# Kernel optimization log

Hardware: AMD Instinct MI355X
Metric: run time of the kernel (lower is better)

The kernel has to match this reference:

```python
import jax, jax.numpy as jnp
import numpy as np

E, T_MAX, H, L, V = 384, 256, 6, 6, 65
DH = E // H  # 64
EPS = 1e-5


def setup_inputs() -> dict:
    key = jax.random.key(0)
    ks = jax.random.split(key, 24)
    B, T = 128, 256
    s = 0.02
    inp = {
        "input_indices": jax.random.randint(ks[0], (B, T), 0, V, dtype=jnp.int64) if jax.config.read("jax_enable_x64") else jax.random.randint(ks[0], (B, T), 0, V, dtype=jnp.int32),
        "targets": jax.random.randint(ks[1], (B, T), 0, V, dtype=jnp.int32),
        "tok_emb": s * jax.random.normal(ks[2], (V, E), jnp.float32),
        "pos_emb": s * jax.random.normal(ks[3], (T_MAX, E), jnp.float32),
        "Wq": s * jax.random.normal(ks[4], (L, H, E, DH), jnp.float32),
        "Wk": s * jax.random.normal(ks[5], (L, H, E, DH), jnp.float32),
        "Wv": s * jax.random.normal(ks[6], (L, H, E, DH), jnp.float32),
        "Wo": s * jax.random.normal(ks[7], (L, E, E), jnp.float32),
        "bo": jnp.zeros((L, E), jnp.float32),
        "ln1_s": jnp.ones((L, E), jnp.float32),
        "ln1_b": jnp.zeros((L, E), jnp.float32),
        "ln2_s": jnp.ones((L, E), jnp.float32),
        "ln2_b": jnp.zeros((L, E), jnp.float32),
        "W1": s * jax.random.normal(ks[8], (L, E, 4 * E), jnp.float32),
        "b1": jnp.zeros((L, 4 * E), jnp.float32),
        "W2": s * jax.random.normal(ks[9], (L, 4 * E, E), jnp.float32),
        "b2": jnp.zeros((L, E), jnp.float32),
        "lnf_s": jnp.ones((E,), jnp.float32),
        "lnf_b": jnp.zeros((E,), jnp.float32),
        "Wout": s * jax.random.normal(ks[10], (E, V), jnp.float32),
        "bout": jnp.zeros((V,), jnp.float32),
    }
    return inp


def _ln(x, s, b):
    m = x.mean(-1, keepdims=True)
    v = ((x - m) ** 2).mean(-1, keepdims=True)
    return (x - m) * jax.lax.rsqrt(v + EPS) * s + b


def _forward(input_indices, targets, tok_emb, pos_emb, Wq, Wk, Wv, Wo, bo,
             ln1_s, ln1_b, ln2_s, ln2_b, W1, b1, W2, b2, lnf_s, lnf_b, Wout, bout):
    B, T = input_indices.shape
    x = tok_emb[input_indices] + pos_emb[:T]  # [B,T,E]
    causal = jnp.tril(jnp.ones((T, T), bool))
    scale = DH ** -0.5

    def block(x, p):
        wq, wk, wv, wo, bo_, l1s, l1b, l2s, l2b, w1, b1_, w2, b2_ = p
        h = _ln(x, l1s, l1b)
        q = jnp.einsum("bte,hed->bhtd", h, wq)
        k = jnp.einsum("bte,hed->bhtd", h, wk)
        v = jnp.einsum("bte,hed->bhtd", h, wv)
        scores = jnp.einsum("bhtd,bhsd->bhts", q, k) * scale
        scores = jnp.where(causal, scores, -jnp.inf)
        w = jax.nn.softmax(scores, axis=-1)
        att = jnp.einsum("bhts,bhsd->bhtd", w, v)  # [B,H,T,DH]
        att = att.transpose(0, 2, 1, 3).reshape(B, T, E)  # concat heads
        x = x + att @ wo + bo_
        h2 = _ln(x, l2s, l2b)
        ff = jax.nn.relu(h2 @ w1 + b1_) @ w2 + b2_
        return x + ff, None

    x, _ = jax.lax.scan(block, x, (Wq, Wk, Wv, Wo, bo, ln1_s, ln1_b, ln2_s, ln2_b, W1, b1, W2, b2))
    x = _ln(x, lnf_s, lnf_b)
    logits = x @ Wout + bout  # [B,T,V]
    logp = jax.nn.log_softmax(logits, axis=-1)
    nll = -jnp.take_along_axis(logp, targets[..., None], axis=-1)[..., 0]
    loss = nll.mean()
    return logits, loss


def reference(input_indices, targets, tok_emb, pos_emb, Wq, Wk, Wv, Wo, bo,
              ln1_s, ln1_b, ln2_s, ln2_b, W1, b1, W2, b2, lnf_s, lnf_b, Wout, bout):
    return _forward(input_indices, targets, tok_emb, pos_emb, Wq, Wk, Wv, Wo, bo,
                    ln1_s, ln1_b, ln2_s, ln2_b, W1, b1, W2, b2, lnf_s, lnf_b, Wout, bout)
```

## Files before the change

### kernel.cpp

```cpp
#include <hip/hip_runtime.h>

#define BT      32768
#define T_SEQ   256
#define E_DIM   384
#define NH      6
#define NL      6
#define VOC     65
#define FF_DIM  1536
#define QKV_N   1152

typedef short bf16x8 __attribute__((ext_vector_type(8)));
typedef float f32x4  __attribute__((ext_vector_type(4)));
typedef unsigned short u16;

typedef const unsigned int __attribute__((address_space(1))) gu32;
typedef unsigned int       __attribute__((address_space(3))) lu32;

__device__ __forceinline__ u16 f2bf(float x) {
  unsigned u = __builtin_bit_cast(unsigned, x);
  u += 0x7fffu + ((u >> 16) & 1u);
  return (u16)(u >> 16);
}
__device__ __forceinline__ float bf2f(u16 v) {
  unsigned u = ((unsigned)v) << 16;
  return __builtin_bit_cast(float, u);
}

__device__ __forceinline__ void load_lds_16(const void* g, void* l) {
  __builtin_amdgcn_global_load_lds((gu32*)g, (lu32*)l, 16, 0, 0);
}

__global__ __launch_bounds__(256) void transpose_t(
    const float* __restrict__ src, u16* __restrict__ dst, int R, int C,
    long sbs, long dbs_outer, int inner, long dbs_inner, long dbase) {
  __shared__ float t[32][33];
  const int b = blockIdx.z;
  const float* s = src + (long)b * sbs;
  u16* d = dst + dbase + (long)(b / inner) * dbs_outer + (long)(b % inner) * dbs_inner;
  const int r0 = blockIdx.x * 32, c0 = blockIdx.y * 32;
  const int tx = threadIdx.x & 31, ty = threadIdx.x >> 5;
#pragma unroll
  for (int i = 0; i < 4; i++) {
    int rr = ty + i * 8;
    int r = r0 + rr, c = c0 + tx;
    if (r < R && c < C) t[rr][tx] = s[(long)r * C + c];
  }
  __syncthreads();
#pragma unroll
  for (int i = 0; i < 4; i++) {
    int cc = ty + i * 8;
    int c = c0 + cc, r = r0 + tx;
    if (c < C && r < R) d[(long)c * R + r] = f2bf(t[tx][cc]);
  }
}

__global__ __launch_bounds__(256) void embed_k(const int* __restrict__ idx,
                                               const float* __restrict__ tok,
                                               const float* __restrict__ pos,
                                               u16* __restrict__ x) {
  int i = blockIdx.x * 256 + threadIdx.x;
  int bt = i / 48, q = i - bt * 48;
  int t = bt & 255;
  const float4* tp = (const float4*)(tok + (size_t)idx[bt] * E_DIM + q * 8);
  const float4* pp = (const float4*)(pos + (size_t)t * E_DIM + q * 8);
  float4 a0 = tp[0], a1 = tp[1], p0 = pp[0], p1 = pp[1];
  u16 o[8];
  o[0] = f2bf(a0.x + p0.x); o[1] = f2bf(a0.y + p0.y);
  o[2] = f2bf(a0.z + p0.z); o[3] = f2bf(a0.w + p0.w);
  o[4] = f2bf(a1.x + p1.x); o[5] = f2bf(a1.y + p1.y);
  o[6] = f2bf(a1.z + p1.z); o[7] = f2bf(a1.w + p1.w);
  *(bf16x8*)(x + (size_t)bt * E_DIM + q * 8) = *(bf16x8*)o;
}

__global__ __launch_bounds__(256) void ln_k(const u16* __restrict__ x,
                                            const float* __restrict__ gam,
                                            const float* __restrict__ bet,
                                            u16* __restrict__ out) {
  int tid = threadIdx.x, lane = tid & 63, w = tid >> 6;
  size_t token = (size_t)blockIdx.x * 4 + w;
  const u16* xr = x + token * E_DIM;
  u16 raw[6];
  *(uint2*)raw          = *(const uint2*)(xr + 4 * lane);
  *(unsigned*)(raw + 4) = *(const unsigned*)(xr + 256 + 2 * lane);
  float v[6]; float s = 0.f;
#pragma unroll
  for (int i = 0; i < 6; i++) { v[i] = bf2f(raw[i]); s += v[i]; }
#pragma unroll
  for (int d = 1; d < 64; d <<= 1) s += __shfl_xor(s, d);
  float mean = s * (1.f / E_DIM);
  float q = 0.f;
#pragma unroll
  for (int i = 0; i < 6; i++) { float d0 = v[i] - mean; q += d0 * d0; }
#pragma unroll
  for (int d = 1; d < 64; d <<= 1) q += __shfl_xor(q, d);
  float r = rsqrtf(q * (1.f / E_DIM) + 1e-5f);
  int e[6] = {4 * lane, 4 * lane + 1, 4 * lane + 2, 4 * lane + 3,
              256 + 2 * lane, 256 + 2 * lane + 1};
  u16 o[6];
#pragma unroll
  for (int i = 0; i < 6; i++)
    o[i] = f2bf((v[i] - mean) * r * gam[e[i]] + bet[e[i]]);
  u16* orow = out + token * E_DIM;
  *(uint2*)(orow + 4 * lane)          = *(uint2*)o;
  *(unsigned*)(orow + 256 + 2 * lane) = *(unsigned*)(o + 4);
}

__global__ __launch_bounds__(256) void gemm_d(
    const u16* __restrict__ A, const u16* __restrict__ Bt, int K, int Nstore,
    const float* __restrict__ bias, const u16* __restrict__ resid,
    u16* __restrict__ outH, float* __restrict__ outF, int relu) {
  __shared__ u16 smem[16384];
  u16* As = smem;
  u16* Bs = smem + 8192;
  const int tid = threadIdx.x, lane = tid & 63, wv = tid >> 6;
  const int quad = lane >> 4, l16 = lane & 15;
  const int m0 = blockIdx.x * 128, n0 = blockIdx.y * 128;
  const int wm = (wv & 1) * 64, wn = (wv >> 1) * 64;

  const int lrow = lane >> 2;
  const int lchunk = (lane & 3) ^ (lrow & 3);
  const int rs = quad == 0 ? 0 : quad;

  f32x4 acc[4][4];
#pragma unroll
  for (int i = 0; i < 4; i++)
#pragma unroll
    for (int j = 0; j < 4; j++) acc[i][j] = (f32x4){0.f, 0.f, 0.f, 0.f};

  auto stage = [&](int sel, int k0) {
#pragma unroll
    for (int j = 0; j < 2; j++) {
      int rid = wv * 2 + j;
      int r = rid * 16 + lrow;
      load_lds_16(A + (size_t)(m0 + r) * K + k0 + lchunk * 8, &As[sel * 4096 + rid * 512]);
      load_lds_16(Bt + (size_t)(n0 + r) * K + k0 + lchunk * 8, &Bs[sel * 4096 + rid * 512]);
    }
  };

  const int NK = K >> 5;
  stage(0, 0);
  __syncthreads();
  for (int kt = 0; kt < NK; kt++) {
    const int cur = kt & 1;
    if (kt + 1 < NK) stage(cur ^ 1, (kt + 1) * 32);
    const u16* Ab = As + cur * 4096;
    const u16* Bb = Bs + cur * 4096;
    const int slot = (quad ^ (l16 & 3)) * 8;
    bf16x8 af[4], bfr[4];
#pragma unroll
    for (int i = 0; i < 4; i++) af[i]  = *(const bf16x8*)&Ab[(wm + i * 16 + l16) * 32 + slot];
#pragma unroll
    for (int j = 0; j < 4; j++) bfr[j] = *(const bf16x8*)&Bb[(wn + j * 16 + l16) * 32 + slot];
#pragma unroll
    for (int i = 0; i < 4; i++)
#pragma unroll
      for (int j = 0; j < 4; j++)
        acc[i][j] = __builtin_amdgcn_mfma_f32_16x16x32_bf16(af[i], bfr[j], acc[i][j], 0, 0, 0);
    __syncthreads();
  }

  if (outH) {
#pragma unroll
    for (int p = 0; p < 4; p++) {
      if (p) __syncthreads();
      if ((wv >> 1) == (p >> 1)) {
#pragma unroll
        for (int jj = 0; jj < 2; jj++) {
          int j = (p & 1) * 2 + jj;
          int gn = n0 + wn + j * 16 + l16;
          float bv = bias ? bias[gn] : 0.f;
          int lcol = jj * 16 + l16;
#pragma unroll
          for (int i = 0; i < 4; i++)
#pragma unroll
            for (int r = 0; r < 4; r++) {
              float v = acc[i][j][r] + bv;
              if (relu) v = fmaxf(v, 0.f);
              smem[(wm + i * 16 + quad * 4 + r) * 36 + lcol] = f2bf(v);
            }
        }
      }
      __syncthreads();
      const int gc0 = n0 + p * 32;
#pragma unroll
      for (int s = 0; s < 4; s++) {
        int row = s * 32 + (tid >> 3);
        int seg = (tid & 7) * 4;
        u16 pk[4];
        *(uint2*)pk = *(const uint2*)&smem[row * 36 + seg];
        size_t o = (size_t)(m0 + row) * Nstore + gc0 + seg;
        if (resid) {
          u16 rv[4];
          *(uint2*)rv = *(const uint2*)&resid[o];
#pragma unroll
          for (int q2 = 0; q2 < 4; q2++) pk[q2] = f2bf(bf2f(pk[q2]) + bf2f(rv[q2]));
        }
        *(uint2*)&outH[o] = *(uint2*)pk;
      }
    }
  } else {
#pragma unroll
    for (int j = 0; j < 4; j++) {
      const int gn = n0 + wn + j * 16 + l16;
      if (gn < Nstore) {
        const float bv = bias ? bias[gn] : 0.f;
#pragma unroll
        for (int i = 0; i < 4; i++)
#pragma unroll
          for (int r = 0; r < 4; r++) {
            const int gm = m0 + wm + i * 16 + quad * 4 + r;
            outF[(size_t)gm * Nstore + gn] = acc[i][j][r] + bv;
          }
      }
    }
  }
}

__global__ __launch_bounds__(512) void attn_k(const u16* __restrict__ qkv,
                                              u16* __restrict__ att) {
  __shared__ u16 Kc[64 * 64];
  __shared__ u16 Vtc[64 * 64];
  __shared__ u16 Pl[8 * 32 * 64];
  const int b = blockIdx.x / NH, h = blockIdx.x % NH;
  const int tid = threadIdx.x, lane = tid & 63, w = tid >> 6;
  const int quad = lane >> 4, l16 = lane & 15;
  const int rowb = b * T_SEQ;

  bf16x8 qf[2][2];
#pragma unroll
  for (int mi = 0; mi < 2; mi++)
#pragma unroll
    for (int kk = 0; kk < 2; kk++)
      qf[mi][kk] = *(const bf16x8*)(qkv + (size_t)(rowb + w * 32 + mi * 16 + l16) * QKV_N +
                                    h * 64 + kk * 32 + quad * 8);

  f32x4 Oa[2][4];
  float mrun[2][4], lrun[2][4];
#pragma unroll
  for (int mi = 0; mi < 2; mi++) {
#pragma unroll
    for (int di = 0; di < 4; di++) Oa[mi][di] = (f32x4){0.f, 0.f, 0.f, 0.f};
#pragma unroll
    for (int r = 0; r < 4; r++) { mrun[mi][r] = -1e30f; lrun[mi][r] = 0.f; }
  }

  u16* Pw = &Pl[w * 2048];
  const int nch = (w >> 1) + 1;
  const int sr = tid >> 3, sseg = (tid & 7) * 8;

  for (int c = 0; c < 4; c++) {
    const int s0 = c * 64;
    __syncthreads();
    *(uint4*)&Kc[sr * 64 + sseg] =
        *(const uint4*)(qkv + (size_t)(rowb + s0 + sr) * QKV_N + 384 + h * 64 + sseg);
    {
      union { uint4 u; u16 us[8]; } tb;
      tb.u = *(const uint4*)(qkv + (size_t)(rowb + s0 + sr) * QKV_N + 768 + h * 64 + sseg);
#pragma unroll
      for (int j = 0; j < 8; j++) Vtc[(sseg + j) * 64 + sr] = tb.us[j];
    }
    __syncthreads();
    if (c >= nch) continue;

    f32x4 S[2][4];
    bf16x8 kf[4][2];
#pragma unroll
    for (int ni = 0; ni < 4; ni++)
#pragma unroll
      for (int kk = 0; kk < 2; kk++)
        kf[ni][kk] = *(const bf16x8*)&Kc[(ni * 16 + l16) * 64 + kk * 32 + quad * 8];
#pragma unroll
    for (int mi = 0; mi < 2; mi++)
#pragma unroll
      for (int ni = 0; ni < 4; ni++) {
        f32x4 z = (f32x4){0.f, 0.f, 0.f, 0.f};
        z = __builtin_amdgcn_mfma_f32_16x16x32_bf16(qf[mi][0], kf[ni][0], z, 0, 0, 0);
        S[mi][ni] = __builtin_amdgcn_mfma_f32_16x16x32_bf16(qf[mi][1], kf[ni][1], z, 0, 0, 0);
      }
    const bool diag = (c == nch - 1);
#pragma unroll
    for (int mi = 0; mi < 2; mi++)
#pragma unroll
      for (int ni = 0; ni < 4; ni++)
#pragma unroll
        for (int r = 0; r < 4; r++) {
          float xv = S[mi][ni][r] * 0.125f;
          if (diag) {
            int t = w * 32 + mi * 16 + quad * 4 + r;
            int s = s0 + ni * 16 + l16;
            if (s > t) xv = -1e30f;
          }
          S[mi][ni][r] = xv;
        }
#pragma unroll
    for (int mi = 0; mi < 2; mi++)
#pragma unroll
      for (int r = 0; r < 4; r++) {
        float mx = fmaxf(fmaxf(S[mi][0][r], S[mi][1][r]), fmaxf(S[mi][2][r], S[mi][3][r]));
        mx = fmaxf(mx, __shfl_xor(mx, 1));
        mx = fmaxf(mx, __shfl_xor(mx, 2));
        mx = fmaxf(mx, __shfl_xor(mx, 4));
        mx = fmaxf(mx, __shfl_xor(mx, 8));
        float mnew = fmaxf(mrun[mi][r], mx);
        float alpha = __expf(mrun[mi][r] - mnew);
        float ls = 0.f;
#pragma unroll
        for (int ni = 0; ni < 4; ni++) {
          float p = __expf(S[mi][ni][r] - mnew);
          S[mi][ni][r] = p; ls += p;
        }
        ls += __shfl_xor(ls, 1); ls += __shfl_xor(ls, 2);
        ls += __shfl_xor(ls, 4); ls += __shfl_xor(ls, 8);
        lrun[mi][r] = lrun[mi][r] * alpha + ls;
        mrun[mi][r] = mnew;
#pragma unroll
        for (int di = 0; di < 4; di++) Oa[mi][di][r] *= alpha;
      }
#pragma unroll
    for (int mi = 0; mi < 2; mi++)
#pragma unroll
      for (int ni = 0; ni < 4; ni++)
#pragma unroll
        for (int r = 0; r < 4; r++)
          Pw[(mi * 16 + quad * 4 + r) * 64 + ni * 16 + l16] = f2bf(S[mi][ni][r]);
    bf16x8 pf[2][2], vf[4][2];
#pragma unroll
    for (int mi = 0; mi < 2; mi++)
#pragma unroll
      for (int kk = 0; kk < 2; kk++)
        pf[mi][kk] = *(const bf16x8*)&Pw[(mi * 16 + l16) * 64 + kk * 32 + quad * 8];
#pragma unroll
    for (int di = 0; di < 4; di++)
#pragma unroll
      for (int kk = 0; kk < 2; kk++)
        vf[di][kk] = *(const bf16x8*)&Vtc[(di * 16 + l16) * 64 + kk * 32 + quad * 8];
#pragma unroll
    for (int mi = 0; mi < 2; mi++)
#pragma unroll
      for (int di = 0; di < 4; di++) {
        Oa[mi][di] = __builtin_amdgcn_mfma_f32_16x16x32_bf16(pf[mi][0], vf[di][0], Oa[mi][di], 0, 0, 0);
        Oa[mi][di] = __builtin_amdgcn_mfma_f32_16x16x32_bf16(pf[mi][1], vf[di][1], Oa[mi][di], 0, 0, 0);
      }
  }

#pragma unroll
  for (int mi = 0; mi < 2; mi++)
#pragma unroll
    for (int r = 0; r < 4; r++) {
      float inv = 1.f / lrun[mi][r];
      int t = w * 32 + mi * 16 + quad * 4 + r;
#pragma unroll
      for (int di = 0; di < 4; di++)
        att[(size_t)(rowb + t) * E_DIM + h * 64 + di * 16 + l16] = f2bf(Oa[mi][di][r] * inv);
    }
}

__global__ __launch_bounds__(256) void loss_k(const float* __restrict__ logits,
                                              const int* __restrict__ tgt,
                                              float* __restrict__ loss) {
  __shared__ float part[4];
  const int tid = threadIdx.x, lane = tid & 63, w = tid >> 6;
  const int wave_id = blockIdx.x * 4 + w;
  float acc = 0.f;
  for (int t = wave_id; t < BT; t += 2048) {
    const float* row = logits + (size_t)t * VOC;
    float a = row[lane];
    float b = (lane == 0) ? row[64] : -1e30f;
    float mx = fmaxf(a, b);
#pragma unroll
    for (int d = 1; d < 64; d <<= 1) mx = fmaxf(mx, __shfl_xor(mx, d));
    float sum = __expf(a - mx) + ((lane == 0) ? __expf(b - mx) : 0.f);
#pragma unroll
    for (int d = 1; d < 64; d <<= 1) sum += __shfl_xor(sum, d);
    if (lane == 0) acc += mx + __logf(sum) - row[tgt[t]];
  }
  if (lane == 0) part[w] = acc;
  __syncthreads();
  if (tid == 0)
    atomicAdd(loss, (part[0] + part[1] + part[2] + part[3]) * (1.f / (float)BT));
}

extern "C" void kernel_launch(void* const* d_in, const int* in_sizes, int n_in,
                              void* d_out, int out_size, void* d_ws, size_t ws_size,
                              hipStream_t stream) {
  (void)in_sizes; (void)n_in; (void)out_size; (void)ws_size;
  const int*   idx  = (const int*)d_in[0];
  const int*   tgt  = (const int*)d_in[1];
  const float* tok  = (const float*)d_in[2];
  const float* pos  = (const float*)d_in[3];
  const float* Wq   = (const float*)d_in[4];
  const float* Wk   = (const float*)d_in[5];
  const float* Wv   = (const float*)d_in[6];
  const float* Wo   = (const float*)d_in[7];
  const float* bo   = (const float*)d_in[8];
  const float* ln1s = (const float*)d_in[9];
  const float* ln1b = (const float*)d_in[10];
  const float* ln2s = (const float*)d_in[11];
  const float* ln2b = (const float*)d_in[12];
  const float* W1   = (const float*)d_in[13];
  const float* b1   = (const float*)d_in[14];
  const float* W2   = (const float*)d_in[15];
  const float* b2   = (const float*)d_in[16];
  const float* lnfs = (const float*)d_in[17];
  const float* lnfb = (const float*)d_in[18];
  const float* Wout = (const float*)d_in[19];
  const float* bout = (const float*)d_in[20];

  char* w = (char*)d_ws;
  u16* x      = (u16*)w;    w += (size_t)BT * E_DIM * 2;
  u16* hb     = (u16*)w;    w += (size_t)BT * E_DIM * 2;
  u16* attb   = (u16*)w;    w += (size_t)BT * E_DIM * 2;
  u16* big    = (u16*)w;    w += (size_t)BT * FF_DIM * 2;
  u16* Wqkv_t = (u16*)w;    w += (size_t)NL * QKV_N * E_DIM * 2;
  u16* Wo_t   = (u16*)w;    w += (size_t)NL * E_DIM * E_DIM * 2;
  u16* W1_t   = (u16*)w;    w += (size_t)NL * FF_DIM * E_DIM * 2;
  u16* W2_t   = (u16*)w;    w += (size_t)NL * E_DIM * FF_DIM * 2;
  u16* Wout_t = (u16*)w;    w += (size_t)128 * E_DIM * 2;
  u16* qkv = big;
  u16* ff  = big;

  float* logits = (float*)d_out;
  float* loss   = logits + (size_t)BT * VOC;

  hipMemsetAsync(Wout_t, 0, 128 * E_DIM * 2, stream);
  transpose_t<<<dim3(12, 2, 36), 256, 0, stream>>>(Wq, Wqkv_t, 384, 64,
      24576, 442368, 6, 24576, 0);
  transpose_t<<<dim3(12, 2, 36), 256, 0, stream>>>(Wk, Wqkv_t, 384, 64,
      24576, 442368, 6, 24576, (long)384 * 384);
  transpose_t<<<dim3(12, 2, 36), 256, 0, stream>>>(Wv, Wqkv_t, 384, 64,
      24576, 442368, 6, 24576, (long)768 * 384);
  transpose_t<<<dim3(12, 12, 6), 256, 0, stream>>>(Wo, Wo_t, 384, 384,
      147456, 147456, 1, 0, 0);
  transpose_t<<<dim3(12, 48, 6), 256, 0, stream>>>(W1, W1_t, 384, 1536,
      589824, 589824, 1, 0, 0);
  transpose_t<<<dim3(48, 12, 6), 256, 0, stream>>>(W2, W2_t, 1536, 384,
      589824, 589824, 1, 0, 0);
  transpose_t<<<dim3(12, 3, 1), 256, 0, stream>>>(Wout, Wout_t, 384, 65,
      0, 0, 1, 0, 0);

  embed_k<<<6144, 256, 0, stream>>>(idx, tok, pos, x);

  for (int l = 0; l < NL; l++) {
    ln_k<<<8192, 256, 0, stream>>>(x, ln1s + l * E_DIM, ln1b + l * E_DIM, hb);
    gemm_d<<<dim3(256, 9), 256, 0, stream>>>(hb, Wqkv_t + (size_t)l * QKV_N * E_DIM,
                                             384, QKV_N, nullptr, nullptr, qkv, nullptr, 0);
    attn_k<<<768, 512, 0, stream>>>(qkv, attb);
    gemm_d<<<dim3(256, 3), 256, 0, stream>>>(attb, Wo_t + (size_t)l * E_DIM * E_DIM,
                                             384, E_DIM, bo + l * E_DIM, x, x, nullptr, 0);
    ln_k<<<8192, 256, 0, stream>>>(x, ln2s + l * E_DIM, ln2b + l * E_DIM, hb);
    gemm_d<<<dim3(256, 12), 256, 0, stream>>>(hb, W1_t + (size_t)l * FF_DIM * E_DIM,
                                              384, FF_DIM, b1 + l * FF_DIM, nullptr, ff, nullptr, 1);
    gemm_d<<<dim3(256, 3), 256, 0, stream>>>(ff, W2_t + (size_t)l * E_DIM * FF_DIM,
                                             1536, E_DIM, b2 + l * E_DIM, x, x, nullptr, 0);
  }
  ln_k<<<8192, 256, 0, stream>>>(x, lnfs, lnfb, hb);
  gemm_d<<<dim3(256, 1), 256, 0, stream>>>(hb, Wout_t, 384, VOC, bout, nullptr, nullptr, logits, 0);

  hipMemsetAsync(loss, 0, 4, stream);
  loss_k<<<512, 256, 0, stream>>>(logits, tgt, loss);
}
```

Before: 1.801 ms.

## Balance causal attention across waves and swizzle LDS layouts to avoid bank conflicts

Attention now gives each wave a pair of 16-row query tiles (w and 15-w), so the causal work is spread evenly instead of later waves doing up to four times the chunks of earlier ones. K, transposed V and P tiles in LDS use XOR swizzles to cut bank conflicts, and the P scratch shrinks to 16 rows per wave. The GEMM's LDS swizzle key changes to a different row bit pattern, and the slot computation moves out of the k loop. The risks are higher register pressure and index arithmetic, and the swizzle must match on both the write and the read side.

```diff
diff --git a/kernel.cpp b/kernel.cpp
--- a/kernel.cpp
+++ b/kernel.cpp
@@ -118,8 +118,7 @@
   const int wm = (wv & 1) * 64, wn = (wv >> 1) * 64;
 
   const int lrow = lane >> 2;
-  const int lchunk = (lane & 3) ^ (lrow & 3);
-  const int rs = quad == 0 ? 0 : quad;
+  const int lchunk = (lane & 3) ^ ((lane >> 3) & 3);
 
   f32x4 acc[4][4];
 #pragma unroll
@@ -140,12 +139,12 @@
   const int NK = K >> 5;
   stage(0, 0);
   __syncthreads();
+  const int slot = (quad ^ ((l16 >> 1) & 3)) * 8;
   for (int kt = 0; kt < NK; kt++) {
     const int cur = kt & 1;
     if (kt + 1 < NK) stage(cur ^ 1, (kt + 1) * 32);
     const u16* Ab = As + cur * 4096;
     const u16* Bb = Bs + cur * 4096;
-    const int slot = (quad ^ (l16 & 3)) * 8;
     bf16x8 af[4], bfr[4];
 #pragma unroll
     for (int i = 0; i < 4; i++) af[i]  = *(const bf16x8*)&Ab[(wm + i * 16 + l16) * 32 + slot];
@@ -220,138 +219,146 @@
                                               u16* __restrict__ att) {
   __shared__ u16 Kc[64 * 64];
   __shared__ u16 Vtc[64 * 64];
-  __shared__ u16 Pl[8 * 32 * 64];
+  __shared__ u16 Pl[8 * 16 * 64];
   const int b = blockIdx.x / NH, h = blockIdx.x % NH;
   const int tid = threadIdx.x, lane = tid & 63, w = tid >> 6;
   const int quad = lane >> 4, l16 = lane & 15;
   const int rowb = b * T_SEQ;
+  const int tiles[2] = {w, 15 - w};
 
   bf16x8 qf[2][2];
 #pragma unroll
-  for (int mi = 0; mi < 2; mi++)
+  for (int ti = 0; ti < 2; ti++)
 #pragma unroll
     for (int kk = 0; kk < 2; kk++)
-      qf[mi][kk] = *(const bf16x8*)(qkv + (size_t)(rowb + w * 32 + mi * 16 + l16) * QKV_N +
+      qf[ti][kk] = *(const bf16x8*)(qkv + (size_t)(rowb + tiles[ti] * 16 + l16) * QKV_N +
                                     h * 64 + kk * 32 + quad * 8);
 
   f32x4 Oa[2][4];
   float mrun[2][4], lrun[2][4];
 #pragma unroll
-  for (int mi = 0; mi < 2; mi++) {
-#pragma unroll
-    for (int di = 0; di < 4; di++) Oa[mi][di] = (f32x4){0.f, 0.f, 0.f, 0.f};
-#pragma unroll
-    for (int r = 0; r < 4; r++) { mrun[mi][r] = -1e30f; lrun[mi][r] = 0.f; }
-  }
-
-  u16* Pw = &Pl[w * 2048];
-  const int nch = (w >> 1) + 1;
-  const int sr = tid >> 3, sseg = (tid & 7) * 8;
+  for (int ti = 0; ti < 2; ti++) {
+#pragma unroll
+    for (int di = 0; di < 4; di++) Oa[ti][di] = (f32x4){0.f, 0.f, 0.f, 0.f};
+#pragma unroll
+    for (int r = 0; r < 4; r++) { mrun[ti][r] = -1e30f; lrun[ti][r] = 0.f; }
+  }
+
+  u16* Pw = &Pl[w * 1024];
+  const int sr = tid >> 3, sseg = tid & 7;
+  const int kst = sseg ^ (sr & 7) ^ ((sr >> 3) & 7);
 
   for (int c = 0; c < 4; c++) {
     const int s0 = c * 64;
     __syncthreads();
-    *(uint4*)&Kc[sr * 64 + sseg] =
-        *(const uint4*)(qkv + (size_t)(rowb + s0 + sr) * QKV_N + 384 + h * 64 + sseg);
+    *(uint4*)&Kc[sr * 64 + kst * 8] =
+        *(const uint4*)(qkv + (size_t)(rowb + s0 + sr) * QKV_N + 384 + h * 64 + sseg * 8);
     {
       union { uint4 u; u16 us[8]; } tb;
-      tb.u = *(const uint4*)(qkv + (size_t)(rowb + s0 + sr) * QKV_N + 768 + h * 64 + sseg);
-#pragma unroll
-      for (int j = 0; j < 8; j++) Vtc[(sseg + j) * 64 + sr] = tb.us[j];
+      tb.u = *(const uint4*)(qkv + (size_t)(rowb + s0 + sr) * QKV_N + 768 + h * 64 + sseg * 8);
+#pragma unroll
+      for (int j = 0; j < 8; j++) {
+        int d = sseg * 8 + j;
+        int vst = (sr >> 3) ^ (d & 7) ^ ((d >> 3) & 7);
+        Vtc[d * 64 + vst * 8 + (sr & 7)] = tb.us[j];
+      }
     }
     __syncthreads();
-    if (c >= nch) continue;
-
-    f32x4 S[2][4];
-    bf16x8 kf[4][2];
-#pragma unroll
-    for (int ni = 0; ni < 4; ni++)
-#pragma unroll
-      for (int kk = 0; kk < 2; kk++)
-        kf[ni][kk] = *(const bf16x8*)&Kc[(ni * 16 + l16) * 64 + kk * 32 + quad * 8];
-#pragma unroll
-    for (int mi = 0; mi < 2; mi++)
+
+    bf16x8 kf[4][2], vf[4][2];
+    bool loaded = false;
+#pragma unroll
+    for (int ti = 0; ti < 2; ti++) {
+      const int t = tiles[ti];
+      if (t < 4 * c) continue;
+      if (!loaded) {
+        loaded = true;
+#pragma unroll
+        for (int ni = 0; ni < 4; ni++)
+#pragma unroll
+          for (int kk = 0; kk < 2; kk++) {
+            int srow = ni * 16 + l16;
+            int ks = (kk * 4 + quad) ^ (srow & 7) ^ ((srow >> 3) & 7);
+            kf[ni][kk] = *(const bf16x8*)&Kc[srow * 64 + ks * 8];
+            int drow = ni * 16 + l16;
+            int vs = (kk * 4 + quad) ^ (drow & 7) ^ ((drow >> 3) & 7);
+            vf[ni][kk] = *(const bf16x8*)&Vtc[drow * 64 + vs * 8];
+          }
+      }
+      f32x4 S[4];
 #pragma unroll
       for (int ni = 0; ni < 4; ni++) {
         f32x4 z = (f32x4){0.f, 0.f, 0.f, 0.f};
-        z = __builtin_amdgcn_mfma_f32_16x16x32_bf16(qf[mi][0], kf[ni][0], z, 0, 0, 0);
-        S[mi][ni] = __builtin_amdgcn_mfma_f32_16x16x32_bf16(qf[mi][1], kf[ni][1], z, 0, 0, 0);
-      }
-    const bool diag = (c == nch - 1);
-#pragma unroll
-    for (int mi = 0; mi < 2; mi++)
+        z = __builtin_amdgcn_mfma_f32_16x16x32_bf16(qf[ti][0], kf[ni][0], z, 0, 0, 0);
+        S[ni] = __builtin_amdgcn_mfma_f32_16x16x32_bf16(qf[ti][1], kf[ni][1], z, 0, 0, 0);
+      }
+      const bool diag = ((t >> 2) == c);
 #pragma unroll
       for (int ni = 0; ni < 4; ni++)
 #pragma unroll
         for (int r = 0; r < 4; r++) {
-          float xv = S[mi][ni][r] * 0.125f;
+          float xv = S[ni][r] * 0.125f;
           if (diag) {
-            int t = w * 32 + mi * 16 + quad * 4 + r;
+            int trow = t * 16 + quad * 4 + r;
             int s = s0 + ni * 16 + l16;
-            if (s > t) xv = -1e30f;
+            if (s > trow) xv = -1e30f;
           }
-          S[mi][ni][r] = xv;
+          S[ni][r] = xv;
         }
 #pragma unroll
-    for (int mi = 0; mi < 2; mi++)
-#pragma unroll
       for (int r = 0; r < 4; r++) {
-        float mx = fmaxf(fmaxf(S[mi][0][r], S[mi][1][r]), fmaxf(S[mi][2][r], S[mi][3][r]));
+        float mx = fmaxf(fmaxf(S[0][r], S[1][r]), fmaxf(S[2][r], S[3][r]));
         mx = fmaxf(mx, __shfl_xor(mx, 1));
         mx = fmaxf(mx, __shfl_xor(mx, 2));
         mx = fmaxf(mx, __shfl_xor(mx, 4));
         mx = fmaxf(mx, __shfl_xor(mx, 8));
-        float mnew = fmaxf(mrun[mi][r], mx);
-        float alpha = __expf(mrun[mi][r] - mnew);
+        float mnew = fmaxf(mrun[ti][r], mx);
+        float alpha = __expf(mrun[ti][r] - mnew);
         float ls = 0.f;
 #pragma unroll
         for (int ni = 0; ni < 4; ni++) {
-          float p = __expf(S[mi][ni][r] - mnew);
-          S[mi][ni][r] = p; ls += p;
+          float p = __expf(S[ni][r] - mnew);
+          S[ni][r] = p; ls += p;
         }
         ls += __shfl_xor(ls, 1); ls += __shfl_xor(ls, 2);
         ls += __shfl_xor(ls, 4); ls += __shfl_xor(ls, 8);
-        lrun[mi][r] = lrun[mi][r] * alpha + ls;
-        mrun[mi][r] = mnew;
-#pragma unroll
-        for (int di = 0; di < 4; di++) Oa[mi][di][r] *= alpha;
-      }
-#pragma unroll
-    for (int mi = 0; mi < 2; mi++)
+        lrun[ti][r] = lrun[ti][r] * alpha + ls;
+        mrun[ti][r] = mnew;
+#pragma unroll
+        for (int di = 0; di < 4; di++) Oa[ti][di][r] *= alpha;
+      }
 #pragma unroll
       for (int ni = 0; ni < 4; ni++)
 #pragma unroll
-        for (int r = 0; r < 4; r++)
-          Pw[(mi * 16 + quad * 4 + r) * 64 + ni * 16 + l16] = f2bf(S[mi][ni][r]);
-    bf16x8 pf[2][2], vf[4][2];
-#pragma unroll
-    for (int mi = 0; mi < 2; mi++)
-#pragma unroll
-      for (int kk = 0; kk < 2; kk++)
-        pf[mi][kk] = *(const bf16x8*)&Pw[(mi * 16 + l16) * 64 + kk * 32 + quad * 8];
-#pragma unroll
-    for (int di = 0; di < 4; di++)
-#pragma unroll
-      for (int kk = 0; kk < 2; kk++)
-        vf[di][kk] = *(const bf16x8*)&Vtc[(di * 16 + l16) * 64 + kk * 32 + quad * 8];
-#pragma unroll
-    for (int mi = 0; mi < 2; mi++)
+        for (int r = 0; r < 4; r++) {
+          int ch = 2 * ni + (l16 >> 3);
+          int st = ch ^ (quad | ((r & 1) << 2));
+          Pw[(quad * 4 + r) * 64 + st * 8 + (l16 & 7)] = f2bf(S[ni][r]);
+        }
+      bf16x8 pf[2];
+#pragma unroll
+      for (int kk = 0; kk < 2; kk++) {
+        int key = (l16 >> 2) | ((l16 & 1) << 2);
+        int st = (kk * 4 + quad) ^ key;
+        pf[kk] = *(const bf16x8*)&Pw[l16 * 64 + st * 8];
+      }
 #pragma unroll
       for (int di = 0; di < 4; di++) {
-        Oa[mi][di] = __builtin_amdgcn_mfma_f32_16x16x32_bf16(pf[mi][0], vf[di][0], Oa[mi][di], 0, 0, 0);
-        Oa[mi][di] = __builtin_amdgcn_mfma_f32_16x16x32_bf16(pf[mi][1], vf[di][1], Oa[mi][di], 0, 0, 0);
-      }
-  }
-
-#pragma unroll
-  for (int mi = 0; mi < 2; mi++)
+        Oa[ti][di] = __builtin_amdgcn_mfma_f32_16x16x32_bf16(pf[0], vf[di][0], Oa[ti][di], 0, 0, 0);
+        Oa[ti][di] = __builtin_amdgcn_mfma_f32_16x16x32_bf16(pf[1], vf[di][1], Oa[ti][di], 0, 0, 0);
+      }
+    }
+  }
+
+#pragma unroll
+  for (int ti = 0; ti < 2; ti++)
 #pragma unroll
     for (int r = 0; r < 4; r++) {
-      float inv = 1.f / lrun[mi][r];
-      int t = w * 32 + mi * 16 + quad * 4 + r;
+      float inv = 1.f / lrun[ti][r];
+      int trow = tiles[ti] * 16 + quad * 4 + r;
 #pragma unroll
       for (int di = 0; di < 4; di++)
-        att[(size_t)(rowb + t) * E_DIM + h * 64 + di * 16 + l16] = f2bf(Oa[mi][di][r] * inv);
+        att[(size_t)(rowb + trow) * E_DIM + h * 64 + di * 16 + l16] = f2bf(Oa[ti][di][r] * inv);
     }
 }
 
```

Result: no change. 1.800 ms (-0.1%).
